# Kernel tuning notes

Measured on AMD Instinct MI355X. Metric: run time of the kernel, lower is better.

## Reference

```python
import jax, jax.numpy as jnp
import numpy as np

L, B, T, H = 3, 128, 256, 512  # layers, batch, seq_max_len, n_hidden


def setup_inputs() -> dict:
    key = jax.random.key(0)
    k0, k1, k2 = jax.random.split(key, 3)
    scale = 1.0 / np.sqrt(H).astype(np.float32)
    x = jax.random.normal(k0, (B, T, H), jnp.float32)
    kernels = jax.random.normal(k1, (L, H, 3 * H), jnp.float32) * scale
    rec_kernels = jax.random.normal(k2, (L, H, 3 * H), jnp.float32) * scale
    biases = jnp.zeros((L, 2, 3 * H), jnp.float32)  # [input_bias, recurrent_bias] (reset_after=True)
    return {"x": x, "kernels": kernels, "rec_kernels": rec_kernels, "biases": biases}


def _gru_layer(x, h0, Wk, Wu, b):
    # x: [B,T,D], h0: [B,H], Wk: [D,3H], Wu: [H,3H], b: [2,3H]
    # Keras GRU, reset_after=True, gate order (z, r, h)
    xp = jnp.einsum('btd,dh->bth', x, Wk) + b[0]  # precompute input projections
    br = b[1]

    def step(h, xp_t):
        rec = h @ Wu + br                      # [B,3H]
        xz, xr, xh = jnp.split(xp_t, 3, axis=-1)
        rz, rr, rh = jnp.split(rec, 3, axis=-1)
        z = jax.nn.sigmoid(xz + rz)
        r = jax.nn.sigmoid(xr + rr)
        hh = jnp.tanh(xh + r * rh)
        h_new = z * h + (1.0 - z) * hh
        return h_new, h_new

    last_h, seq = jax.lax.scan(step, h0, jnp.swapaxes(xp, 0, 1))  # seq: [T,B,H]
    return jnp.swapaxes(seq, 0, 1), last_h


def reference(x, kernels, rec_kernels, biases):
    Bc, Tc, _ = x.shape
    Hd = kernels.shape[2] // 3
    state = None
    for l in range(kernels.shape[0]):
        # layer l>0 receives previous layer's final state as initial_state
        h0 = jnp.zeros((Bc, Hd), x.dtype) if state is None else state
        x, state = _gru_layer(x, h0, kernels[l], rec_kernels[l], biases[l])
    # tf.reshape(states, (-1, H)) then tf.split(seq_max_len, axis=0) -> stack == reshape to [T, B, H]
    states_h = x.reshape(-1, Hd).reshape(Tc, -1, Hd)
    return states_h, state
```

## Files before the change

### kernel.cpp

```cpp
#include <hip/hip_runtime.h>
#include <hip/hip_bf16.h>

#define NL  3
#define NB  128
#define NT  256
#define NH  512
#define NH3 1536
#define NBH (NB*NH)
#define NM  (NB*NT)

typedef __bf16 bf16x8 __attribute__((ext_vector_type(8)));
typedef float  floatx4 __attribute__((ext_vector_type(4)));
typedef int    intx4  __attribute__((ext_vector_type(4)));
typedef __hip_bfloat16 bf16;
typedef unsigned long long u64;

__device__ __forceinline__ floatx4 mfma16(bf16x8 a, bf16x8 b, floatx4 c) {
  return __builtin_amdgcn_mfma_f32_16x16x32_bf16(a, b, c, 0, 0, 0);
}
__device__ __forceinline__ void gload16(const void* g, void* l) {
  __builtin_amdgcn_global_load_lds(
      (const __attribute__((address_space(1))) unsigned int*)g,
      (__attribute__((address_space(3))) unsigned int*)l, 16, 0, 0);
}
__device__ __forceinline__ float fsig(float x)  { return 1.0f / (1.0f + __expf(-x)); }
__device__ __forceinline__ float ftanh(float x) { return 2.0f / (1.0f + __expf(-2.0f*x)) - 1.0f; }
__device__ __forceinline__ float b2f(unsigned short u) {
  unsigned v = (unsigned)u << 16; float f; __builtin_memcpy(&f, &v, 4); return f;
}
__device__ __forceinline__ unsigned short f2b(float f) {
  bf16 h = __float2bfloat16(f); unsigned short u; __builtin_memcpy(&u, &h, 2); return u;
}
__device__ __forceinline__ u64 ald(const u64* p) {
  return __hip_atomic_load(p, __ATOMIC_RELAXED, __HIP_MEMORY_SCOPE_AGENT);
}
__device__ __forceinline__ void ast(u64* p, u64 v) {
  __hip_atomic_store(p, v, __ATOMIC_RELAXED, __HIP_MEMORY_SCOPE_AGENT);
}

__device__ __forceinline__ void ld64(const void* p, intx4& a, intx4& b, intx4& c, intx4& d) {
  asm volatile(
      "global_load_dwordx4 %0, %4, off sc1\n\t"
      "global_load_dwordx4 %1, %4, off offset:16 sc1\n\t"
      "global_load_dwordx4 %2, %4, off offset:32 sc1\n\t"
      "global_load_dwordx4 %3, %4, off offset:48 sc1\n\t"
      "s_waitcnt vmcnt(0)"
      : "=&v"(a), "=&v"(b), "=&v"(c), "=&v"(d)
      : "v"(p)
      : "memory");
}

__global__ void transpose_cvt_kernel(const float* __restrict__ in, bf16* __restrict__ out) {
  __shared__ float tile[32][33];
  int l = blockIdx.z;
  int n0 = blockIdx.x * 32, k0 = blockIdx.y * 32;
  const float* src = in + (size_t)l * NH * NH3;
  bf16* dst = out + (size_t)l * NH3 * NH;
  int tx = threadIdx.x, ty = threadIdx.y;
#pragma unroll
  for (int i = 0; i < 4; i++)
    tile[ty + 8*i][tx] = src[(size_t)(k0 + ty + 8*i) * NH3 + n0 + tx];
  __syncthreads();
#pragma unroll
  for (int i = 0; i < 4; i++)
    dst[(size_t)(n0 + ty + 8*i) * NH + k0 + tx] = __float2bfloat16(tile[tx][ty + 8*i]);
}

__global__ void cvt_x_kernel(const float* __restrict__ in, bf16* __restrict__ out) {
  size_t i = (size_t)blockIdx.x * blockDim.x + threadIdx.x;
  float4 v = ((const float4*)in)[i];
  ushort4 pk;
  pk.x = f2b(v.x); pk.y = f2b(v.y); pk.z = f2b(v.z); pk.w = f2b(v.w);
  ((ushort4*)out)[i] = pk;
}

__global__ void __launch_bounds__(256, 2) gemm_xp_kernel(
    const bf16* __restrict__ A, const bf16* __restrict__ Bt,
    const float* __restrict__ bias, bf16* __restrict__ C, int a_mode)
{
  __shared__ char alds[16384];
  __shared__ char blds[16384];
  int tid = threadIdx.x;
  int lane = tid & 63, w = tid >> 6;
  int mblk = blockIdx.x, nblk = blockIdx.y;
  int wm = w >> 1, wn = w & 1;
  int klane = (lane >> 4) * 8;
  int r0 = 2*w*16 + (lane & 15);
  size_t arow0, arow1;
  if (a_mode == 0) {
    arow0 = ((size_t)r0 * NT + mblk) * NH;
    arow1 = ((size_t)(r0 + 16) * NT + mblk) * NH;
  } else {
    arow0 = (size_t)(mblk*128 + r0) * NH;
    arow1 = arow0 + (size_t)16 * NH;
  }
  size_t brow0 = (size_t)(nblk*128 + 2*w*16 + (lane & 15)) * NH;
  size_t brow1 = brow0 + (size_t)16 * NH;

  floatx4 acc[4][4];
#pragma unroll
  for (int i = 0; i < 4; i++)
#pragma unroll
    for (int j = 0; j < 4; j++) acc[i][j] = (floatx4){0.f, 0.f, 0.f, 0.f};

  for (int kk = 0; kk < 8; kk++) {
    int kb = kk*64 + klane;
#pragma unroll
    for (int kt = 0; kt < 2; kt++) {
      int kg = kb + kt*32;
      gload16(A  + arow0 + kg, alds + (kt*8 + 2*w    ) * 1024);
      gload16(A  + arow1 + kg, alds + (kt*8 + 2*w + 1) * 1024);
      gload16(Bt + brow0 + kg, blds + (kt*8 + 2*w    ) * 1024);
      gload16(Bt + brow1 + kg, blds + (kt*8 + 2*w + 1) * 1024);
    }
    __syncthreads();
#pragma unroll
    for (int kt = 0; kt < 2; kt++) {
      bf16x8 af[4], bfr[4];
#pragma unroll
      for (int i = 0; i < 4; i++) af[i]  = *(const bf16x8*)(alds + ((kt*8 + wm*4 + i)*64 + lane)*16);
#pragma unroll
      for (int j = 0; j < 4; j++) bfr[j] = *(const bf16x8*)(blds + ((kt*8 + wn*4 + j)*64 + lane)*16);
#pragma unroll
      for (int i = 0; i < 4; i++)
#pragma unroll
        for (int j = 0; j < 4; j++)
          acc[i][j] = mfma16(af[i], bfr[j], acc[i][j]);
    }
    __syncthreads();
  }
  int cl = lane & 15, rbase = (lane >> 4) * 4;
#pragma unroll
  for (int i = 0; i < 4; i++) {
    int gm = mblk*128 + wm*64 + i*16 + rbase;
#pragma unroll
    for (int j = 0; j < 4; j++) {
      int gn = nblk*128 + wn*64 + j*16 + cl;
      float bv = bias[gn];
#pragma unroll
      for (int r = 0; r < 4; r++)
        C[(size_t)(gm + r) * NH3 + gn] = __float2bfloat16(acc[i][j][r] + bv);
    }
  }
}

__global__ void __launch_bounds__(512, 2) gru_scan_kernel(
    const bf16*  __restrict__ wuT,
    const float* __restrict__ br,
    const bf16*  __restrict__ xp,
    bf16*        __restrict__ seq,
    float*       __restrict__ hlast,
    float*       __restrict__ out,
    u64*         __restrict__ xbuf,
    unsigned tagbase, int layer)
{
  __shared__ __align__(16) char h_raw[2][16384];
  __shared__ volatile int deadflag;
  int tid = threadIdx.x, lane = tid & 63, w = tid >> 6;
  int g = blockIdx.x >> 2, c = blockIdx.x & 3;
  int bb0 = g * 16;
  int r16 = lane & 15, h4 = lane >> 4;
  int srow = tid & 15, ssc = tid >> 4;
  if (tid == 0) deadflag = 0;

  bf16x8 wf[3][16];
  float  bv[3][4];
#pragma unroll
  for (int G = 0; G < 3; G++) {
    const bf16* wrow = wuT + ((size_t)(G*NH + c*128 + w*16 + r16)) * NH + h4*8;
#pragma unroll
    for (int kt = 0; kt < 16; kt++) wf[G][kt] = *(const bf16x8*)(wrow + kt*32);
#pragma unroll
    for (int q = 0; q < 4; q++) bv[G][q] = br[G*NH + c*128 + w*16 + h4*4 + q];
  }

  float hreg[4];
  if (layer == 0) {
    hreg[0] = hreg[1] = hreg[2] = hreg[3] = 0.0f;
  } else {
    const float* hsrc = hlast + (size_t)(bb0 + r16) * NH + c*128 + w*16 + h4*4;
    float4 v = *(const float4*)hsrc;
    hreg[0] = v.x; hreg[1] = v.y; hreg[2] = v.z; hreg[3] = v.w;
  }

  u64* seqU = (u64*)seq;
  const size_t PARU = (size_t)8 * 512 * 8;
  u64* pubp = xbuf + (size_t)g*4096 + ((size_t)((w*4 + h4)*16 + r16))*8 + (size_t)(c*2);
  bool fastok = true;

  for (int t = 0; t < NT; t++) {
    if (t == 0) {
      if (layer == 0) {
        *(int4*)(h_raw[0] + tid*32)      = (int4){0,0,0,0};
        *(int4*)(h_raw[0] + tid*32 + 16) = (int4){0,0,0,0};
      } else {
        const u64* src = seqU + ((size_t)NT*NBH + (size_t)(bb0 + srow)*NH) / 4;
#pragma unroll
        for (int d = 0; d < 2; d++) {
          int sc = ssc + d*32;
          u64 q0 = ald(src + sc*2), q1 = ald(src + sc*2 + 1);
          u64* dst = (u64*)(h_raw[0] + (((sc >> 2)*64) + (sc & 3)*16 + srow)*16);
          dst[0] = q0; dst[1] = q1;
        }
      }
    } else {
      const u64* sb = xbuf + (size_t)(t & 1)*PARU + (size_t)g*4096 + (size_t)tid*8;
      unsigned want = tagbase + (unsigned)t;
      int w_ = (int)want;
      u64 q0 = 0, q1 = 0, q2 = 0, q3 = 0;
      bool got = false;
      if (fastok) {
        for (int it = 0; it < 8; ++it) {
          intx4 A, B2, C2, D2;
          ld64(sb, A, B2, C2, D2);
          if (A.y == w_ && A.w == w_ && B2.y == w_ && B2.w == w_ &&
              C2.y == w_ && C2.w == w_ && D2.y == w_ && D2.w == w_) {
            q0 = (u64)(unsigned)A.x  | ((u64)(unsigned)A.z  << 32);
            q1 = (u64)(unsigned)B2.x | ((u64)(unsigned)B2.z << 32);
            q2 = (u64)(unsigned)C2.x | ((u64)(unsigned)C2.z << 32);
            q3 = (u64)(unsigned)D2.x | ((u64)(unsigned)D2.z << 32);
            got = true; break;
          }
        }
        if (!got) fastok = false;
      }
      if (!got) {
        int it = 0;
        while (!deadflag) {
          u64 a0 = ald(sb+0), a1 = ald(sb+1), b0 = ald(sb+2), b1 = ald(sb+3);
          u64 c0 = ald(sb+4), c1 = ald(sb+5), d0 = ald(sb+6), d1 = ald(sb+7);
          bool ok = ((unsigned)(a0 >> 32) == want) & ((unsigned)(a1 >> 32) == want) &
                    ((unsigned)(b0 >> 32) == want) & ((unsigned)(b1 >> 32) == want) &
                    ((unsigned)(c0 >> 32) == want) & ((unsigned)(c1 >> 32) == want) &
                    ((unsigned)(d0 >> 32) == want) & ((unsigned)(d1 >> 32) == want);
          if (ok) {
            q0 = (u64)(unsigned)a0 | ((u64)(unsigned)a1 << 32);
            q1 = (u64)(unsigned)b0 | ((u64)(unsigned)b1 << 32);
            q2 = (u64)(unsigned)c0 | ((u64)(unsigned)c1 << 32);
            q3 = (u64)(unsigned)d0 | ((u64)(unsigned)d1 << 32);
            break;
          }
          if (++it > (1 << 17)) { deadflag = 1; break; }
        }
      }
      char* hb = h_raw[t & 1];
      int j0 = ssc, j1 = ssc + 32, j2 = ssc + 64, j3 = ssc + 96;
      *(u64*)(hb + (((j0>>3)*64 + ((j0>>1)&3)*16 + srow)*16 + (j0&1)*8)) = q0;
      *(u64*)(hb + (((j1>>3)*64 + ((j1>>1)&3)*16 + srow)*16 + (j1&1)*8)) = q1;
      *(u64*)(hb + (((j2>>3)*64 + ((j2>>1)&3)*16 + srow)*16 + (j2&1)*8)) = q2;
      *(u64*)(hb + (((j3>>3)*64 + ((j3>>1)&3)*16 + srow)*16 + (j3&1)*8)) = q3;
    }

    const u64* xq = (const u64*)(xp + ((size_t)t*NB + bb0 + r16)*NH3 + c*128 + w*16 + h4*4);
    u64 xv0 = xq[0], xv1 = xq[128], xv2 = xq[256];

    __syncthreads();

    const char* hbR = h_raw[t & 1];
    floatx4 ac0 = (floatx4){0,0,0,0}, ac1 = (floatx4){0,0,0,0}, ac2 = (floatx4){0,0,0,0};
#pragma unroll
    for (int kt = 0; kt < 16; kt++) {
      bf16x8 hb = *(const bf16x8*)(hbR + (kt*64 + lane)*16);
      ac0 = mfma16(wf[0][kt], hb, ac0);
      ac1 = mfma16(wf[1][kt], hb, ac1);
      ac2 = mfma16(wf[2][kt], hb, ac2);
    }

    unsigned short pk[4];
#pragma unroll
    for (int q = 0; q < 4; q++) {
      float rz = ac0[q] + bv[0][q];
      float rr = ac1[q] + bv[1][q];
      float rh = ac2[q] + bv[2][q];
      float xz = b2f((unsigned short)(xv0 >> (16*q)));
      float xr = b2f((unsigned short)(xv1 >> (16*q)));
      float xh = b2f((unsigned short)(xv2 >> (16*q)));
      float z  = fsig(xz + rz);
      float r  = fsig(xr + rr);
      float hh = ftanh(xh + r * rh);
      float hn = z * hreg[q] + (1.0f - z) * hh;
      hreg[q] = hn;
      pk[q] = f2b(hn);
    }
    u64 pv; __builtin_memcpy(&pv, pk, 8);

    if (t < NT - 1) {
      u64 tg = (u64)(tagbase + (unsigned)t + 1u) << 32;
      u64* pp = pubp + (size_t)((t + 1) & 1) * PARU;
      ast(pp,     ((u64)(unsigned)(pv & 0xffffffffu)) | tg);
      ast(pp + 1, ((u64)(unsigned)(pv >> 32))         | tg);
    }
    if (layer != 2)
      seqU[((size_t)(t+1)*NBH + (size_t)(bb0 + r16)*NH)/4 + c*32 + w*4 + h4] = pv;

    if (layer == 2) {
      float* o = out + ((size_t)(bb0 + r16)*NT + t)*NH + c*128 + w*16 + h4*4;
      *(float4*)o = (float4){hreg[0], hreg[1], hreg[2], hreg[3]};
      if (t == NT - 1) {
        float* o2 = out + (size_t)NM*NH + (size_t)(bb0 + r16)*NH + c*128 + w*16 + h4*4;
        *(float4*)o2 = (float4){hreg[0], hreg[1], hreg[2], hreg[3]};
      }
    } else if (t == NT - 1) {
      float* o = hlast + (size_t)(bb0 + r16)*NH + c*128 + w*16 + h4*4;
      *(float4*)o = (float4){hreg[0], hreg[1], hreg[2], hreg[3]};
    }
  }
}

extern "C" void kernel_launch(void* const* d_in, const int* in_sizes, int n_in,
                              void* d_out, int out_size, void* d_ws, size_t ws_size,
                              hipStream_t stream) {
  const float* x   = (const float*)d_in[0];
  const float* wk  = (const float*)d_in[1];
  const float* wu  = (const float*)d_in[2];
  const float* bis = (const float*)d_in[3];
  float* out = (float*)d_out;

  const size_t REQ = 144572416;
  if (ws_size < REQ) {
    hipMemsetAsync(d_out, 0, (size_t)out_size * 4, stream);
    return;
  }
  char* ws = (char*)d_ws;
  bf16*  wkT   = (bf16*)(ws);
  bf16*  wuT   = (bf16*)(ws + 4718592);
  bf16*  xp    = (bf16*)(ws + 9437184);
  bf16*  seq   = (bf16*)(ws + 110100480);
  bf16*  xb    = seq;
  float* hlast = (float*)(ws + 143785984);
  u64*   xbuf  = (u64*)(ws + 144048128);

  hipMemsetAsync(xbuf, 0, 524288, stream);
  transpose_cvt_kernel<<<dim3(48,16,3), dim3(32,8), 0, stream>>>(wk, wkT);
  transpose_cvt_kernel<<<dim3(48,16,3), dim3(32,8), 0, stream>>>(wu, wuT);
  cvt_x_kernel<<<(NM*NH/4)/256, 256, 0, stream>>>(x, xb);

  const size_t WS = (size_t)NH3 * NH;

  gemm_xp_kernel<<<dim3(256,12), 256, 0, stream>>>(xb, wkT, bis + 0*2*NH3, xp, 0);
  gru_scan_kernel<<<32, 512, 0, stream>>>(wuT, bis + 0*2*NH3 + NH3, xp,
      seq, hlast, nullptr, xbuf, 0u, 0);
  gemm_xp_kernel<<<dim3(256,12), 256, 0, stream>>>(seq + NBH, wkT + WS, bis + 1*2*NH3, xp, 1);
  gru_scan_kernel<<<32, 512, 0, stream>>>(wuT + WS, bis + 1*2*NH3 + NH3, xp,
      seq, hlast, nullptr, xbuf, 256u, 1);
  gemm_xp_kernel<<<dim3(256,12), 256, 0, stream>>>(seq + NBH, wkT + 2*WS, bis + 2*2*NH3, xp, 1);
  gru_scan_kernel<<<32, 512, 0, stream>>>(wuT + 2*WS, bis + 2*2*NH3 + NH3, xp,
      seq, hlast, out, xbuf, 512u, 2);

  (void)in_sizes; (void)n_in; (void)out_size; (void)ws_size;
}
```

Measured before the change: 3.868 ms.

## Split inter-block exchange into fast sc0 buffer and atomic fallback buffer

The per-step hidden-state exchange between cooperating blocks now writes each value twice: once as a single 16-byte store into a fast buffer, polled with sc0 vector loads, and once as relaxed atomics into a separate fallback buffer. The fast poll gets more retries, and the block-to-group mapping changes so that the four column blocks of a batch group are spread across block IDs. The aim is to cut synchronisation latency on the serial recurrence. In exchange it adds an extra store per step and relies on sc0 loads seeing other CUs' writes without stale-cache issues, which the atomic fallback guards against.

```diff
diff --git a/kernel.cpp b/kernel.cpp
--- a/kernel.cpp
+++ b/kernel.cpp
@@ -38,12 +38,12 @@
   __hip_atomic_store(p, v, __ATOMIC_RELAXED, __HIP_MEMORY_SCOPE_AGENT);
 }
 
-__device__ __forceinline__ void ld64(const void* p, intx4& a, intx4& b, intx4& c, intx4& d) {
+__device__ __forceinline__ void ld64sc0(const void* p, intx4& a, intx4& b, intx4& c, intx4& d) {
   asm volatile(
-      "global_load_dwordx4 %0, %4, off sc1\n\t"
-      "global_load_dwordx4 %1, %4, off offset:16 sc1\n\t"
-      "global_load_dwordx4 %2, %4, off offset:32 sc1\n\t"
-      "global_load_dwordx4 %3, %4, off offset:48 sc1\n\t"
+      "global_load_dwordx4 %0, %4, off sc0\n\t"
+      "global_load_dwordx4 %1, %4, off offset:16 sc0\n\t"
+      "global_load_dwordx4 %2, %4, off offset:32 sc0\n\t"
+      "global_load_dwordx4 %3, %4, off offset:48 sc0\n\t"
       "s_waitcnt vmcnt(0)"
       : "=&v"(a), "=&v"(b), "=&v"(c), "=&v"(d)
       : "v"(p)
@@ -151,13 +151,14 @@
     bf16*        __restrict__ seq,
     float*       __restrict__ hlast,
     float*       __restrict__ out,
-    u64*         __restrict__ xbuf,
+    u64*         __restrict__ abuf,
+    u64*         __restrict__ fbuf,
     unsigned tagbase, int layer)
 {
   __shared__ __align__(16) char h_raw[2][16384];
   __shared__ volatile int deadflag;
   int tid = threadIdx.x, lane = tid & 63, w = tid >> 6;
-  int g = blockIdx.x >> 2, c = blockIdx.x & 3;
+  int g = blockIdx.x & 7, c = blockIdx.x >> 3;
   int bb0 = g * 16;
   int r16 = lane & 15, h4 = lane >> 4;
   int srow = tid & 15, ssc = tid >> 4;
@@ -185,7 +186,7 @@
 
   u64* seqU = (u64*)seq;
   const size_t PARU = (size_t)8 * 512 * 8;
-  u64* pubp = xbuf + (size_t)g*4096 + ((size_t)((w*4 + h4)*16 + r16))*8 + (size_t)(c*2);
+  size_t puboff = (size_t)g*4096 + ((size_t)((w*4 + h4)*16 + r16))*8 + (size_t)(c*2);
   bool fastok = true;
 
   for (int t = 0; t < NT; t++) {
@@ -204,15 +205,16 @@
         }
       }
     } else {
-      const u64* sb = xbuf + (size_t)(t & 1)*PARU + (size_t)g*4096 + (size_t)tid*8;
+      size_t coff = (size_t)(t & 1)*PARU + (size_t)g*4096 + (size_t)tid*8;
       unsigned want = tagbase + (unsigned)t;
       int w_ = (int)want;
       u64 q0 = 0, q1 = 0, q2 = 0, q3 = 0;
       bool got = false;
       if (fastok) {
-        for (int it = 0; it < 8; ++it) {
+        const u64* fb = fbuf + coff;
+        for (int it = 0; it < 32; ++it) {
           intx4 A, B2, C2, D2;
-          ld64(sb, A, B2, C2, D2);
+          ld64sc0(fb, A, B2, C2, D2);
           if (A.y == w_ && A.w == w_ && B2.y == w_ && B2.w == w_ &&
               C2.y == w_ && C2.w == w_ && D2.y == w_ && D2.w == w_) {
             q0 = (u64)(unsigned)A.x  | ((u64)(unsigned)A.z  << 32);
@@ -225,6 +227,7 @@
         if (!got) fastok = false;
       }
       if (!got) {
+        const u64* sb = abuf + coff;
         int it = 0;
         while (!deadflag) {
           u64 a0 = ald(sb+0), a1 = ald(sb+1), b0 = ald(sb+2), b1 = ald(sb+3);
@@ -285,8 +288,16 @@
     u64 pv; __builtin_memcpy(&pv, pk, 8);
 
     if (t < NT - 1) {
-      u64 tg = (u64)(tagbase + (unsigned)t + 1u) << 32;
-      u64* pp = pubp + (size_t)((t + 1) & 1) * PARU;
+      unsigned ptag = tagbase + (unsigned)t + 1u;
+      size_t poff = puboff + (size_t)((t + 1) & 1) * PARU;
+      intx4 pub;
+      pub.x = (int)(unsigned)(pv & 0xffffffffu);
+      pub.y = (int)ptag;
+      pub.z = (int)(unsigned)(pv >> 32);
+      pub.w = (int)ptag;
+      *(intx4*)(fbuf + poff) = pub;
+      u64 tg = (u64)ptag << 32;
+      u64* pp = abuf + poff;
       ast(pp,     ((u64)(unsigned)(pv & 0xffffffffu)) | tg);
       ast(pp + 1, ((u64)(unsigned)(pv >> 32))         | tg);
     }
@@ -316,7 +327,7 @@
   const float* bis = (const float*)d_in[3];
   float* out = (float*)d_out;
 
-  const size_t REQ = 144572416;
+  const size_t REQ = 145096704;
   if (ws_size < REQ) {
     hipMemsetAsync(d_out, 0, (size_t)out_size * 4, stream);
     return;
@@ -328,9 +339,10 @@
   bf16*  seq   = (bf16*)(ws + 110100480);
   bf16*  xb    = seq;
   float* hlast = (float*)(ws + 143785984);
-  u64*   xbuf  = (u64*)(ws + 144048128);
-
-  hipMemsetAsync(xbuf, 0, 524288, stream);
+  u64*   abuf  = (u64*)(ws + 144048128);
+  u64*   fbuf  = (u64*)(ws + 144572416);
+
+  hipMemsetAsync(abuf, 0, 1048576, stream);
   transpose_cvt_kernel<<<dim3(48,16,3), dim3(32,8), 0, stream>>>(wk, wkT);
   transpose_cvt_kernel<<<dim3(48,16,3), dim3(32,8), 0, stream>>>(wu, wuT);
   cvt_x_kernel<<<(NM*NH/4)/256, 256, 0, stream>>>(x, xb);
@@ -339,13 +351,13 @@
 
   gemm_xp_kernel<<<dim3(256,12), 256, 0, stream>>>(xb, wkT, bis + 0*2*NH3, xp, 0);
   gru_scan_kernel<<<32, 512, 0, stream>>>(wuT, bis + 0*2*NH3 + NH3, xp,
-      seq, hlast, nullptr, xbuf, 0u, 0);
+      seq, hlast, nullptr, abuf, fbuf, 0u, 0);
   gemm_xp_kernel<<<dim3(256,12), 256, 0, stream>>>(seq + NBH, wkT + WS, bis + 1*2*NH3, xp, 1);
   gru_scan_kernel<<<32, 512, 0, stream>>>(wuT + WS, bis + 1*2*NH3 + NH3, xp,
-      seq, hlast, nullptr, xbuf, 256u, 1);
+      seq, hlast, nullptr, abuf, fbuf, 256u, 1);
   gemm_xp_kernel<<<dim3(256,12), 256, 0, stream>>>(seq + NBH, wkT + 2*WS, bis + 2*2*NH3, xp, 1);
   gru_scan_kernel<<<32, 512, 0, stream>>>(wuT + 2*WS, bis + 2*2*NH3 + NH3, xp,
-      seq, hlast, out, xbuf, 512u, 2);
+      seq, hlast, out, abuf, fbuf, 512u, 2);
 
   (void)in_sizes; (void)n_in; (void)out_size; (void)ws_size;
 }
```

Measured after the change: 4.746 ms. 22.7% more time.
